# Optimization experiments

Measured on AMD Instinct MI355X. Metric: run time of the kernel, lower is better.

Reference implementation:

```python
import jax, jax.numpy as jnp
import numpy as np

B, T, L, H = 32, 16, 2, 1024  # batch, unroll steps, stacked lstm cells, hidden=input size


def setup_inputs() -> dict:
    key = jax.random.key(0)
    ks = jax.random.split(key, 10)
    s = 1.0 / float(np.sqrt(H))  # torch LSTMCell init scale
    x = jax.random.normal(ks[0], (B, H), jnp.float32)
    h0 = jax.random.normal(ks[1], (L, B, H), jnp.float32)
    c0 = jax.random.normal(ks[2], (L, B, H), jnp.float32)
    # binary zoneout masks (1 -> keep previous state), rate 0.5
    h_mask = (jax.random.uniform(ks[3], (T, L, B, H)) < 0.5).astype(jnp.float32)
    c_mask = (jax.random.uniform(ks[4], (T, L, B, H)) < 0.5).astype(jnp.float32)
    labels = jax.random.normal(ks[5], (B, T, H), jnp.float32)
    W_ih = jax.random.uniform(ks[6], (L, 4 * H, H), jnp.float32, -s, s)
    W_hh = jax.random.uniform(ks[7], (L, 4 * H, H), jnp.float32, -s, s)
    b_ih = jax.random.uniform(ks[8], (L, 4 * H), jnp.float32, -s, s)
    b_hh = jax.random.uniform(ks[9], (L, 4 * H), jnp.float32, -s, s)
    return dict(x=x, h0=h0, c0=c0, h_mask=h_mask, c_mask=c_mask, labels=labels,
                W_ih=W_ih, W_hh=W_hh, b_ih=b_ih, b_hh=b_hh)


def _lstm_cell(x, h, c, W_ih, W_hh, b_ih, b_hh):
    # torch.nn.LSTMCell gate order: i, f, g, o
    gates = x @ W_ih.T + b_ih + h @ W_hh.T + b_hh  # (B, 4H)
    i, f, g, o = jnp.split(gates, 4, axis=-1)
    c_new = jax.nn.sigmoid(f) * c + jax.nn.sigmoid(i) * jnp.tanh(g)
    h_new = jax.nn.sigmoid(o) * jnp.tanh(c_new)
    return h_new, c_new


def reference(x, h0, c0, h_mask, c_mask, labels, W_ih, W_hh, b_ih, b_hh):
    def step(carry, masks):
        hs, cs, out = carry  # hs/cs: (L,B,H), out: (B,H)
        hm, cm = masks       # (L,B,H) each
        new_h, new_c = [], []
        for l in range(L):  # small fixed layer loop (structurally distinct weights)
            h_cand, c_cand = _lstm_cell(out, hs[l], cs[l], W_ih[l], W_hh[l], b_ih[l], b_hh[l])
            # zoneout: mask==1 keeps previous state
            h_l = hm[l] * hs[l] + (1.0 - hm[l]) * h_cand
            c_l = cm[l] * cs[l] + (1.0 - cm[l]) * c_cand
            new_h.append(h_l)
            new_c.append(c_l)
            out = h_l
        return (jnp.stack(new_h), jnp.stack(new_c), out), out

    _, outs = jax.lax.scan(step, (h0, c0, x), (h_mask, c_mask))  # outs: (T,B,H)
    ret = jnp.transpose(outs, (1, 0, 2))  # (B,T,H) == torch.stack(ret, dim=1)
    loss = jnp.mean((ret - labels) ** 2)  # MSELoss
    return ret, loss
```

## Files before the change

### kernel.cpp

```cpp
#include <hip/hip_runtime.h>

#define NTHR 512

typedef __bf16 bf16x8 __attribute__((ext_vector_type(8)));
typedef float  f32x4  __attribute__((ext_vector_type(4)));
typedef unsigned long long u64;

__device__ __forceinline__ unsigned short f2bf(float f) {
  unsigned int u = __float_as_uint(f);
  return (unsigned short)((u + 0x7fffu + ((u >> 16) & 1u)) >> 16);
}
__device__ __forceinline__ bf16x8 asbf(uint4 u) { return __builtin_bit_cast(bf16x8, u); }
__device__ __forceinline__ uint4 mk4(u64 lo, u64 hi) {
  uint2 l = __builtin_bit_cast(uint2, lo), h = __builtin_bit_cast(uint2, hi);
  return make_uint4(l.x, l.y, h.x, h.y);
}
__device__ __forceinline__ float sigf(float xv) { return 1.0f / (1.0f + __expf(-xv)); }

template <typename T>
__device__ __forceinline__ T ald(const T* p) {
  return __hip_atomic_load(p, __ATOMIC_RELAXED, __HIP_MEMORY_SCOPE_AGENT);
}
template <typename T>
__device__ __forceinline__ void xst(T* p, T v) {
  (void)__hip_atomic_exchange(p, v, __ATOMIC_RELAXED, __HIP_MEMORY_SCOPE_AGENT);
}
__device__ __forceinline__ u64 pkf2(float a, float b) {
  float2 f = make_float2(a, b);
  return __builtin_bit_cast(u64, f);
}

#define WS_OUTB 0
#define WS_HBB  131072
#define WS_XFLG 393216
#define WS_HFLG 655360
#define WS_PS   917504
#define WS_BCB  3014656
#define WS_SSE  3047424

__global__ void prep_kernel(const float* __restrict__ x, const float* __restrict__ h0,
                            const float* __restrict__ bih, const float* __restrict__ bhh,
                            unsigned char* __restrict__ ws)
{
  unsigned short* outb = (unsigned short*)(ws + WS_OUTB);
  unsigned short* hbb  = (unsigned short*)(ws + WS_HBB);
  int*   flg = (int*)(ws + WS_XFLG);
  float* bcb = (float*)(ws + WS_BCB);
  float* sse = (float*)(ws + WS_SSE);

  int gid = blockIdx.x * blockDim.x + threadIdx.x;
  int stride = gridDim.x * blockDim.x;

  for (int i = gid; i < 32768; i += stride) outb[i] = f2bf(x[i]);
  for (int i = gid; i < 65536; i += stride) hbb[i] = f2bf(h0[i]);
  for (int i = gid; i < 8192; i += stride) bcb[i] = bih[i] + bhh[i];
  for (int i = gid; i < 131072; i += stride) flg[i] = 0;
  if (gid == 0) *sse = 0.0f;
}

__global__ void __launch_bounds__(NTHR, 1)
lstm_kernel(const float* __restrict__ Wih, const float* __restrict__ Whh,
            const float* __restrict__ h0c, const float* __restrict__ c0c,
            const float* __restrict__ hmask, const float* __restrict__ cmask,
            const float* __restrict__ labels, float* __restrict__ out,
            unsigned char* __restrict__ ws)
{
  const int tid = threadIdx.x, bid = blockIdx.x;
  const int g = bid >> 1, role = bid & 1;
  const int lane = tid & 63, w = tid >> 6;
  const int mt = w & 1, nt = (w >> 1) & 1, kh = w >> 2;
  const int q = lane >> 4, m0 = lane & 15;

  __shared__ __align__(16) unsigned short As[41 * 1032];
  __shared__ __align__(16) float Cred[2][32][36];

  unsigned short* outb = (unsigned short*)(ws + WS_OUTB);
  unsigned short* hbb  = (unsigned short*)(ws + WS_HBB);
  int*   xflg = (int*)(ws + WS_XFLG);
  int*   hflg = (int*)(ws + WS_HFLG);
  float* PsF  = (float*)(ws + WS_PS);
  const float* bcb = (const float*)(ws + WS_BCB);
  float* sse = (float*)(ws + WS_SSE);

  uint4 w0r[16], w1r[16];
  {
    const int nloc = nt * 16 + m0;
    const size_t wrow = (size_t)((nloc >> 3) * 1024 + g * 8 + (nloc & 7));
    const int kbase = kh * 512 + q * 8;
    const float* b0 = (role ? Whh : Wih) + wrow * 1024 + kbase;
    const float* b1 = b0 + 4194304;
#pragma unroll
    for (int ks = 0; ks < 16; ++ks) {
      float4 a = *(const float4*)(b0 + ks * 32), b = *(const float4*)(b0 + ks * 32 + 4);
      w0r[ks].x = (unsigned int)f2bf(a.x) | ((unsigned int)f2bf(a.y) << 16);
      w0r[ks].y = (unsigned int)f2bf(a.z) | ((unsigned int)f2bf(a.w) << 16);
      w0r[ks].z = (unsigned int)f2bf(b.x) | ((unsigned int)f2bf(b.y) << 16);
      w0r[ks].w = (unsigned int)f2bf(b.z) | ((unsigned int)f2bf(b.w) << 16);
      float4 c = *(const float4*)(b1 + ks * 32), d = *(const float4*)(b1 + ks * 32 + 4);
      w1r[ks].x = (unsigned int)f2bf(c.x) | ((unsigned int)f2bf(c.y) << 16);
      w1r[ks].y = (unsigned int)f2bf(c.z) | ((unsigned int)f2bf(c.w) << 16);
      w1r[ks].z = (unsigned int)f2bf(d.x) | ((unsigned int)f2bf(d.y) << 16);
      w1r[ks].w = (unsigned int)f2bf(d.z) | ((unsigned int)f2bf(d.w) << 16);
    }
  }

  const int m = tid >> 3, jc = tid & 7, col = g * 8 + jc;
  float cs0 = 0.f, hs0 = 0.f, cs1 = 0.f, hs1 = 0.f;
  float bv0[4] = {0, 0, 0, 0}, bv1[4] = {0, 0, 0, 0};
  if (role == 0 && tid < 256) {
    cs0 = c0c[m * 1024 + col];           hs0 = h0c[m * 1024 + col];
    cs1 = c0c[32768 + m * 1024 + col];   hs1 = h0c[32768 + m * 1024 + col];
#pragma unroll
    for (int gt = 0; gt < 4; ++gt) {
      bv0[gt] = bcb[gt * 1024 + col];
      bv1[gt] = bcb[4096 + gt * 1024 + col];
    }
  }

#pragma unroll 1
  for (int ci = 0; ci < 32; ++ci) {
    const int t = ci >> 1, L = ci & 1;

    if (role == 0) {
      float hmv = 0.f, cmv = 0.f, lbv = 0.f;
      if (tid < 256) {
        const int mb = ci * 32768 + m * 1024 + col;
        hmv = hmask[mb]; cmv = cmask[mb];
        if (L == 1) lbv = labels[(m * 16 + t) * 1024 + col];
      }

      if (ci > 0 && tid < 128) {
        while (ald(&xflg[((ci - 1) * 128 + tid) * 16]) < ci)
          __builtin_amdgcn_s_sleep(1);
      }
      if (tid >= 128 && tid < 192) {
        while (ald(&hflg[(ci * 128 + g) * 16]) < ci + 1)
          __builtin_amdgcn_s_sleep(1);
      }
      __syncthreads();

      float psv[4];
      const float* psb = PsF + (size_t)(((t & 1) * 2 + L) * 128 + g) * 1024;
      if (tid < 256) {
#pragma unroll
        for (int gt = 0; gt < 4; ++gt)
          psv[gt] = ald(psb + m * 32 + gt * 8 + jc);
      }

      const unsigned short* asrc = outb + L * 32768;
      u64 av[16];
#pragma unroll
      for (int it = 0; it < 16; ++it) {
        const int u = it * 512 + tid, row = u >> 8, c4 = u & 255;
        av[it] = ald((const u64*)(asrc + row * 1024 + c4 * 4));
      }
#pragma unroll
      for (int it = 0; it < 16; ++it) {
        const int u = it * 512 + tid, row = u >> 8, c4 = u & 255;
        *(u64*)&As[row * 1032 + c4 * 4] = av[it];
      }
      __syncthreads();

      f32x4 acc = {0.f, 0.f, 0.f, 0.f};
#pragma unroll
      for (int ks = 0; ks < 16; ++ks) {
        const int kl = kh * 512 + ks * 32 + q * 8;
        bf16x8 a = asbf(*(const uint4*)&As[(mt * 16 + m0) * 1032 + kl]);
        bf16x8 b = asbf((L == 0) ? w0r[ks] : w1r[ks]);
        acc = __builtin_amdgcn_mfma_f32_16x16x32_bf16(a, b, acc, 0, 0, 0);
      }
#pragma unroll
      for (int i = 0; i < 4; ++i)
        Cred[kh][mt * 16 + q * 4 + i][nt * 16 + m0] = acc[i];
      __syncthreads();

      if (tid < 256) {
        float ga[4];
        if (L == 0) {
#pragma unroll
          for (int gt = 0; gt < 4; ++gt)
            ga[gt] = (Cred[0][m][gt * 8 + jc] + Cred[1][m][gt * 8 + jc]) + psv[gt] + bv0[gt];
        } else {
#pragma unroll
          for (int gt = 0; gt < 4; ++gt)
            ga[gt] = (Cred[0][m][gt * 8 + jc] + Cred[1][m][gt * 8 + jc]) + psv[gt] + bv1[gt];
        }
        const float cp = (L == 0) ? cs0 : cs1;
        const float hp = (L == 0) ? hs0 : hs1;
        const float ii = sigf(ga[0]), ff = sigf(ga[1]);
        const float gv = tanhf(ga[2]), oo = sigf(ga[3]);
        const float cc = ff * cp + ii * gv;
        const float hc = oo * tanhf(cc);
        const float hn = hmv * hp + (1.0f - hmv) * hc;
        const float cn = cmv * cp + (1.0f - cmv) * cc;
        if (L == 0) { cs0 = cn; hs0 = hn; } else { cs1 = cn; hs1 = hn; }

        const float hnp = __shfl_xor(hn, 1);
        if ((tid & 1) == 0) {
          const unsigned int hb =
              (unsigned int)f2bf(hn) | ((unsigned int)f2bf(hnp) << 16);
          xst((unsigned int*)&outb[(L ^ 1) * 32768 + m * 1024 + col], hb);
          xst((unsigned int*)&hbb[(((t + 1) & 1) * 2 + L) * 32768 + m * 1024 + col], hb);
        }
        if (L == 1) {
          out[(m * 16 + t) * 1024 + col] = hn;
          float d = hn - lbv;
          float s = d * d;
#pragma unroll
          for (int off = 32; off > 0; off >>= 1) s += __shfl_down(s, off);
          if ((tid & 63) == 0) atomicAdd(sse, s);
        }
      }
      __syncthreads();
      if (tid == 0) xst(&xflg[(ci * 128 + g) * 16], ci + 1);

    } else {
      if (ci > 1 && tid < 128) {
        while (ald(&xflg[((ci - 2) * 128 + tid) * 16]) < ci - 1)
          __builtin_amdgcn_s_sleep(1);
      }
      __syncthreads();

      const unsigned short* asrc = hbb + ((t & 1) * 2 + L) * 32768;
      u64 av[16];
#pragma unroll
      for (int it = 0; it < 16; ++it) {
        const int u = it * 512 + tid, row = u >> 8, c4 = u & 255;
        av[it] = ald((const u64*)(asrc + row * 1024 + c4 * 4));
      }
#pragma unroll
      for (int it = 0; it < 16; ++it) {
        const int u = it * 512 + tid, row = u >> 8, c4 = u & 255;
        *(u64*)&As[row * 1032 + c4 * 4] = av[it];
      }
      __syncthreads();

      f32x4 acc = {0.f, 0.f, 0.f, 0.f};
#pragma unroll
      for (int ks = 0; ks < 16; ++ks) {
        const int kl = kh * 512 + ks * 32 + q * 8;
        bf16x8 a = asbf(*(const uint4*)&As[(mt * 16 + m0) * 1032 + kl]);
        bf16x8 b = asbf((L == 0) ? w0r[ks] : w1r[ks]);
        acc = __builtin_amdgcn_mfma_f32_16x16x32_bf16(a, b, acc, 0, 0, 0);
      }
#pragma unroll
      for (int i = 0; i < 4; ++i)
        Cred[kh][mt * 16 + q * 4 + i][nt * 16 + m0] = acc[i];
      __syncthreads();

      {
        const int mH = tid >> 4, np = tid & 15;
        const float s0 = Cred[0][mH][2 * np]     + Cred[1][mH][2 * np];
        const float s1 = Cred[0][mH][2 * np + 1] + Cred[1][mH][2 * np + 1];
        float* psb = PsF + (size_t)(((t & 1) * 2 + L) * 128 + g) * 1024;
        xst((u64*)(psb + mH * 32 + 2 * np), pkf2(s0, s1));
      }
      __syncthreads();
      if (tid == 0) xst(&hflg[(ci * 128 + g) * 16], ci + 1);
    }
  }
}

__global__ void fin_kernel(float* __restrict__ out, unsigned char* __restrict__ ws) {
  if (blockIdx.x == 0 && threadIdx.x == 0)
    out[524288] = *(float*)(ws + WS_SSE) * (1.0f / 524288.0f);
}

extern "C" void kernel_launch(void* const* d_in, const int* in_sizes, int n_in,
                              void* d_out, int out_size, void* d_ws, size_t ws_size,
                              hipStream_t stream) {
  (void)in_sizes; (void)n_in; (void)out_size; (void)ws_size;
  const float* x   = (const float*)d_in[0];
  const float* h0  = (const float*)d_in[1];
  const float* c0  = (const float*)d_in[2];
  const float* hm  = (const float*)d_in[3];
  const float* cm  = (const float*)d_in[4];
  const float* lb  = (const float*)d_in[5];
  const float* wih = (const float*)d_in[6];
  const float* whh = (const float*)d_in[7];
  const float* bi  = (const float*)d_in[8];
  const float* bh  = (const float*)d_in[9];
  float* out = (float*)d_out;
  unsigned char* ws = (unsigned char*)d_ws;

  prep_kernel<<<dim3(256), dim3(256), 0, stream>>>(x, h0, bi, bh, ws);
  lstm_kernel<<<dim3(256), dim3(NTHR), 0, stream>>>(wih, whh, h0, c0, hm, cm, lb, out, ws);
  fin_kernel<<<dim3(1), dim3(64), 0, stream>>>(out, ws);
}
```

Before: 382.5 us.

## Assign blocks per layer and fuse input and recurrent GEMMs in-block

Work is split across blocks by layer (L = bid&1) instead of by role (input GEMM vs. recurrent-partial GEMM). Each block keeps both its W_ih and W_hh slices in registers. It computes the recurrent partial for the next step locally into shared memory once all blocks have published h. This removes the global partial-sum buffer and the second flag array, but each block now runs two serial GEMMs per step. Layers 0 and 1 can pipeline as a wavefront, with an extra grid-wide wait before each recurrent GEMM.

Result: faster. 343.1 us (-10.3%).

```diff
diff --git a/kernel.cpp b/kernel.cpp
--- a/kernel.cpp
+++ b/kernel.cpp
@@ -11,10 +11,6 @@
   return (unsigned short)((u + 0x7fffu + ((u >> 16) & 1u)) >> 16);
 }
 __device__ __forceinline__ bf16x8 asbf(uint4 u) { return __builtin_bit_cast(bf16x8, u); }
-__device__ __forceinline__ uint4 mk4(u64 lo, u64 hi) {
-  uint2 l = __builtin_bit_cast(uint2, lo), h = __builtin_bit_cast(uint2, hi);
-  return make_uint4(l.x, l.y, h.x, h.y);
-}
 __device__ __forceinline__ float sigf(float xv) { return 1.0f / (1.0f + __expf(-xv)); }
 
 template <typename T>
@@ -25,37 +21,66 @@
 __device__ __forceinline__ void xst(T* p, T v) {
   (void)__hip_atomic_exchange(p, v, __ATOMIC_RELAXED, __HIP_MEMORY_SCOPE_AGENT);
 }
-__device__ __forceinline__ u64 pkf2(float a, float b) {
-  float2 f = make_float2(a, b);
-  return __builtin_bit_cast(u64, f);
-}
-
-#define WS_OUTB 0
-#define WS_HBB  131072
-#define WS_XFLG 393216
-#define WS_HFLG 655360
-#define WS_PS   917504
-#define WS_BCB  3014656
-#define WS_SSE  3047424
+
+#define WS_HOUT 0
+#define WS_XIN  262144
+#define WS_HI0  327680
+#define WS_HI1  393216
+#define WS_FLG  458752
+#define WS_BCB  720896
+#define WS_SSE  753664
 
 __global__ void prep_kernel(const float* __restrict__ x, const float* __restrict__ h0,
                             const float* __restrict__ bih, const float* __restrict__ bhh,
                             unsigned char* __restrict__ ws)
 {
-  unsigned short* outb = (unsigned short*)(ws + WS_OUTB);
-  unsigned short* hbb  = (unsigned short*)(ws + WS_HBB);
-  int*   flg = (int*)(ws + WS_XFLG);
+  unsigned short* xin = (unsigned short*)(ws + WS_XIN);
+  unsigned short* hi0 = (unsigned short*)(ws + WS_HI0);
+  unsigned short* hi1 = (unsigned short*)(ws + WS_HI1);
+  int*   flg = (int*)(ws + WS_FLG);
   float* bcb = (float*)(ws + WS_BCB);
   float* sse = (float*)(ws + WS_SSE);
 
   int gid = blockIdx.x * blockDim.x + threadIdx.x;
   int stride = gridDim.x * blockDim.x;
 
-  for (int i = gid; i < 32768; i += stride) outb[i] = f2bf(x[i]);
-  for (int i = gid; i < 65536; i += stride) hbb[i] = f2bf(h0[i]);
+  for (int i = gid; i < 32768; i += stride) xin[i] = f2bf(x[i]);
+  for (int i = gid; i < 32768; i += stride) hi0[i] = f2bf(h0[i]);
+  for (int i = gid; i < 32768; i += stride) hi1[i] = f2bf(h0[32768 + i]);
   for (int i = gid; i < 8192; i += stride) bcb[i] = bih[i] + bhh[i];
-  for (int i = gid; i < 131072; i += stride) flg[i] = 0;
+  for (int i = gid; i < 65536; i += stride) flg[i] = 0;
   if (gid == 0) *sse = 0.0f;
+}
+
+__device__ __forceinline__ void stage64k(const unsigned short* __restrict__ src,
+                                         unsigned short* __restrict__ As, int tid) {
+  u64 av[16];
+#pragma unroll
+  for (int it = 0; it < 16; ++it) {
+    const int u = it * 512 + tid, row = u >> 8, c4 = u & 255;
+    av[it] = ald((const u64*)(src + row * 1024 + c4 * 4));
+  }
+#pragma unroll
+  for (int it = 0; it < 16; ++it) {
+    const int u = it * 512 + tid, row = u >> 8, c4 = u & 255;
+    *(u64*)&As[row * 1032 + c4 * 4] = av[it];
+  }
+}
+
+__device__ __forceinline__ void gemm_to_cred(const uint4 (&wreg)[16],
+                                             const unsigned short* __restrict__ As,
+                                             float* __restrict__ Cred,
+                                             int mt, int nt, int kh, int q, int m0) {
+  f32x4 acc = {0.f, 0.f, 0.f, 0.f};
+#pragma unroll
+  for (int ks = 0; ks < 16; ++ks) {
+    const int kl = kh * 512 + ks * 32 + q * 8;
+    bf16x8 a = asbf(*(const uint4*)&As[(mt * 16 + m0) * 1032 + kl]);
+    acc = __builtin_amdgcn_mfma_f32_16x16x32_bf16(a, asbf(wreg[ks]), acc, 0, 0, 0);
+  }
+#pragma unroll
+  for (int i = 0; i < 4; ++i)
+    Cred[kh * (32 * 36) + (mt * 16 + q * 4 + i) * 36 + nt * 16 + m0] = acc[i];
 }
 
 __global__ void __launch_bounds__(NTHR, 1)
@@ -66,197 +91,133 @@
             unsigned char* __restrict__ ws)
 {
   const int tid = threadIdx.x, bid = blockIdx.x;
-  const int g = bid >> 1, role = bid & 1;
+  const int L = bid & 1, g = bid >> 1;
   const int lane = tid & 63, w = tid >> 6;
   const int mt = w & 1, nt = (w >> 1) & 1, kh = w >> 2;
   const int q = lane >> 4, m0 = lane & 15;
 
   __shared__ __align__(16) unsigned short As[41 * 1032];
-  __shared__ __align__(16) float Cred[2][32][36];
-
-  unsigned short* outb = (unsigned short*)(ws + WS_OUTB);
-  unsigned short* hbb  = (unsigned short*)(ws + WS_HBB);
-  int*   xflg = (int*)(ws + WS_XFLG);
-  int*   hflg = (int*)(ws + WS_HFLG);
-  float* PsF  = (float*)(ws + WS_PS);
+  __shared__ __align__(16) float Cred[2 * 32 * 36];
+  __shared__ __align__(16) float Hpart[32][33];
+
+  unsigned short* HOUT = (unsigned short*)(ws + WS_HOUT);
+  unsigned short* XIN  = (unsigned short*)(ws + WS_XIN);
+  unsigned short* HIL  = (unsigned short*)(ws + (L ? WS_HI1 : WS_HI0));
+  int*   flg = (int*)(ws + WS_FLG);
   const float* bcb = (const float*)(ws + WS_BCB);
   float* sse = (float*)(ws + WS_SSE);
 
-  uint4 w0r[16], w1r[16];
+  uint4 wx[16], wh[16];
   {
     const int nloc = nt * 16 + m0;
     const size_t wrow = (size_t)((nloc >> 3) * 1024 + g * 8 + (nloc & 7));
     const int kbase = kh * 512 + q * 8;
-    const float* b0 = (role ? Whh : Wih) + wrow * 1024 + kbase;
-    const float* b1 = b0 + 4194304;
+    const float* bx = Wih + (size_t)L * 4194304 + wrow * 1024 + kbase;
+    const float* bh = Whh + (size_t)L * 4194304 + wrow * 1024 + kbase;
 #pragma unroll
     for (int ks = 0; ks < 16; ++ks) {
-      float4 a = *(const float4*)(b0 + ks * 32), b = *(const float4*)(b0 + ks * 32 + 4);
-      w0r[ks].x = (unsigned int)f2bf(a.x) | ((unsigned int)f2bf(a.y) << 16);
-      w0r[ks].y = (unsigned int)f2bf(a.z) | ((unsigned int)f2bf(a.w) << 16);
-      w0r[ks].z = (unsigned int)f2bf(b.x) | ((unsigned int)f2bf(b.y) << 16);
-      w0r[ks].w = (unsigned int)f2bf(b.z) | ((unsigned int)f2bf(b.w) << 16);
-      float4 c = *(const float4*)(b1 + ks * 32), d = *(const float4*)(b1 + ks * 32 + 4);
-      w1r[ks].x = (unsigned int)f2bf(c.x) | ((unsigned int)f2bf(c.y) << 16);
-      w1r[ks].y = (unsigned int)f2bf(c.z) | ((unsigned int)f2bf(c.w) << 16);
-      w1r[ks].z = (unsigned int)f2bf(d.x) | ((unsigned int)f2bf(d.y) << 16);
-      w1r[ks].w = (unsigned int)f2bf(d.z) | ((unsigned int)f2bf(d.w) << 16);
+      float4 a = *(const float4*)(bx + ks * 32), b = *(const float4*)(bx + ks * 32 + 4);
+      wx[ks].x = (unsigned int)f2bf(a.x) | ((unsigned int)f2bf(a.y) << 16);
+      wx[ks].y = (unsigned int)f2bf(a.z) | ((unsigned int)f2bf(a.w) << 16);
+      wx[ks].z = (unsigned int)f2bf(b.x) | ((unsigned int)f2bf(b.y) << 16);
+      wx[ks].w = (unsigned int)f2bf(b.z) | ((unsigned int)f2bf(b.w) << 16);
+      float4 c = *(const float4*)(bh + ks * 32), d = *(const float4*)(bh + ks * 32 + 4);
+      wh[ks].x = (unsigned int)f2bf(c.x) | ((unsigned int)f2bf(c.y) << 16);
+      wh[ks].y = (unsigned int)f2bf(c.z) | ((unsigned int)f2bf(c.w) << 16);
+      wh[ks].z = (unsigned int)f2bf(d.x) | ((unsigned int)f2bf(d.y) << 16);
+      wh[ks].w = (unsigned int)f2bf(d.z) | ((unsigned int)f2bf(d.w) << 16);
     }
   }
 
   const int m = tid >> 3, jc = tid & 7, col = g * 8 + jc;
-  float cs0 = 0.f, hs0 = 0.f, cs1 = 0.f, hs1 = 0.f;
-  float bv0[4] = {0, 0, 0, 0}, bv1[4] = {0, 0, 0, 0};
-  if (role == 0 && tid < 256) {
-    cs0 = c0c[m * 1024 + col];           hs0 = h0c[m * 1024 + col];
-    cs1 = c0c[32768 + m * 1024 + col];   hs1 = h0c[32768 + m * 1024 + col];
-#pragma unroll
-    for (int gt = 0; gt < 4; ++gt) {
-      bv0[gt] = bcb[gt * 1024 + col];
-      bv1[gt] = bcb[4096 + gt * 1024 + col];
-    }
+  float cs = 0.f, hs = 0.f, bv[4] = {0.f, 0.f, 0.f, 0.f};
+  if (tid < 256) {
+    cs = c0c[L * 32768 + m * 1024 + col];
+    hs = h0c[L * 32768 + m * 1024 + col];
+#pragma unroll
+    for (int gt = 0; gt < 4; ++gt) bv[gt] = bcb[L * 4096 + gt * 1024 + col];
+  }
+
+  stage64k(HIL, As, tid);
+  __syncthreads();
+  gemm_to_cred(wh, As, Cred, mt, nt, kh, q, m0);
+  __syncthreads();
+  {
+    const int idx = tid * 2, mh = idx >> 5, nh = idx & 31;
+    Hpart[mh][nh]     = Cred[mh * 36 + nh]     + Cred[32 * 36 + mh * 36 + nh];
+    Hpart[mh][nh + 1] = Cred[mh * 36 + nh + 1] + Cred[32 * 36 + mh * 36 + nh + 1];
   }
 
 #pragma unroll 1
-  for (int ci = 0; ci < 32; ++ci) {
-    const int t = ci >> 1, L = ci & 1;
-
-    if (role == 0) {
-      float hmv = 0.f, cmv = 0.f, lbv = 0.f;
-      if (tid < 256) {
-        const int mb = ci * 32768 + m * 1024 + col;
-        hmv = hmask[mb]; cmv = cmask[mb];
-        if (L == 1) lbv = labels[(m * 16 + t) * 1024 + col];
+  for (int t = 0; t < 16; ++t) {
+    const int ci = 2 * t + L;
+
+    float hmv = 0.f, cmv = 0.f, lbv = 0.f;
+    if (tid < 256) {
+      const int mb = ci * 32768 + m * 1024 + col;
+      hmv = hmask[mb]; cmv = cmask[mb];
+      if (L == 1) lbv = labels[(m * 16 + t) * 1024 + col];
+    }
+
+    if (ci > 0 && tid < 128) {
+      while (ald(&flg[((ci - 1) * 128 + tid) * 16]) < ci)
+        __builtin_amdgcn_s_sleep(1);
+    }
+    __syncthreads();
+
+    const unsigned short* xsrc = (ci == 0)
+        ? XIN
+        : HOUT + (size_t)((L == 0) ? (2 + ((t - 1) & 1)) : (t & 1)) * 32768;
+    stage64k(xsrc, As, tid);
+    __syncthreads();
+
+    gemm_to_cred(wx, As, Cred, mt, nt, kh, q, m0);
+    __syncthreads();
+
+    if (tid < 256) {
+      float ga[4];
+#pragma unroll
+      for (int gt = 0; gt < 4; ++gt)
+        ga[gt] = Cred[m * 36 + gt * 8 + jc] + Cred[32 * 36 + m * 36 + gt * 8 + jc]
+               + Hpart[m][gt * 8 + jc] + bv[gt];
+      const float ii = sigf(ga[0]), ff = sigf(ga[1]);
+      const float gv = tanhf(ga[2]), oo = sigf(ga[3]);
+      const float cc = ff * cs + ii * gv;
+      const float hc = oo * tanhf(cc);
+      const float hn = hmv * hs + (1.0f - hmv) * hc;
+      const float cn = cmv * cs + (1.0f - cmv) * cc;
+      cs = cn; hs = hn;
+
+      const float hnp = __shfl_xor(hn, 1);
+      if (!(tid & 1)) {
+        const unsigned int hb = (unsigned int)f2bf(hn) | ((unsigned int)f2bf(hnp) << 16);
+        xst((unsigned int*)&HOUT[(size_t)(L * 2 + (t & 1)) * 32768 + m * 1024 + col], hb);
       }
-
-      if (ci > 0 && tid < 128) {
-        while (ald(&xflg[((ci - 1) * 128 + tid) * 16]) < ci)
-          __builtin_amdgcn_s_sleep(1);
+      if (L == 1) {
+        out[(m * 16 + t) * 1024 + col] = hn;
+        float d = hn - lbv;
+        float s = d * d;
+#pragma unroll
+        for (int off = 32; off > 0; off >>= 1) s += __shfl_down(s, off);
+        if ((tid & 63) == 0) atomicAdd(sse, s);
       }
-      if (tid >= 128 && tid < 192) {
-        while (ald(&hflg[(ci * 128 + g) * 16]) < ci + 1)
+    }
+    __syncthreads();
+    if (tid == 0) xst(&flg[(ci * 128 + g) * 16], ci + 1);
+
+    if (t < 15) {
+      if (tid < 128) {
+        while (ald(&flg[(ci * 128 + tid) * 16]) < ci + 1)
           __builtin_amdgcn_s_sleep(1);
       }
       __syncthreads();
-
-      float psv[4];
-      const float* psb = PsF + (size_t)(((t & 1) * 2 + L) * 128 + g) * 1024;
-      if (tid < 256) {
-#pragma unroll
-        for (int gt = 0; gt < 4; ++gt)
-          psv[gt] = ald(psb + m * 32 + gt * 8 + jc);
-      }
-
-      const unsigned short* asrc = outb + L * 32768;
-      u64 av[16];
-#pragma unroll
-      for (int it = 0; it < 16; ++it) {
-        const int u = it * 512 + tid, row = u >> 8, c4 = u & 255;
-        av[it] = ald((const u64*)(asrc + row * 1024 + c4 * 4));
-      }
-#pragma unroll
-      for (int it = 0; it < 16; ++it) {
-        const int u = it * 512 + tid, row = u >> 8, c4 = u & 255;
-        *(u64*)&As[row * 1032 + c4 * 4] = av[it];
-      }
+      stage64k(HOUT + (size_t)(L * 2 + (t & 1)) * 32768, As, tid);
       __syncthreads();
-
-      f32x4 acc = {0.f, 0.f, 0.f, 0.f};
-#pragma unroll
-      for (int ks = 0; ks < 16; ++ks) {
-        const int kl = kh * 512 + ks * 32 + q * 8;
-        bf16x8 a = asbf(*(const uint4*)&As[(mt * 16 + m0) * 1032 + kl]);
-        bf16x8 b = asbf((L == 0) ? w0r[ks] : w1r[ks]);
-        acc = __builtin_amdgcn_mfma_f32_16x16x32_bf16(a, b, acc, 0, 0, 0);
-      }
-#pragma unroll
-      for (int i = 0; i < 4; ++i)
-        Cred[kh][mt * 16 + q * 4 + i][nt * 16 + m0] = acc[i];
+      gemm_to_cred(wh, As, Cred, mt, nt, kh, q, m0);
       __syncthreads();
-
-      if (tid < 256) {
-        float ga[4];
-        if (L == 0) {
-#pragma unroll
-          for (int gt = 0; gt < 4; ++gt)
-            ga[gt] = (Cred[0][m][gt * 8 + jc] + Cred[1][m][gt * 8 + jc]) + psv[gt] + bv0[gt];
-        } else {
-#pragma unroll
-          for (int gt = 0; gt < 4; ++gt)
-            ga[gt] = (Cred[0][m][gt * 8 + jc] + Cred[1][m][gt * 8 + jc]) + psv[gt] + bv1[gt];
-        }
-        const float cp = (L == 0) ? cs0 : cs1;
-        const float hp = (L == 0) ? hs0 : hs1;
-        const float ii = sigf(ga[0]), ff = sigf(ga[1]);
-        const float gv = tanhf(ga[2]), oo = sigf(ga[3]);
-        const float cc = ff * cp + ii * gv;
-        const float hc = oo * tanhf(cc);
-        const float hn = hmv * hp + (1.0f - hmv) * hc;
-        const float cn = cmv * cp + (1.0f - cmv) * cc;
-        if (L == 0) { cs0 = cn; hs0 = hn; } else { cs1 = cn; hs1 = hn; }
-
-        const float hnp = __shfl_xor(hn, 1);
-        if ((tid & 1) == 0) {
-          const unsigned int hb =
-              (unsigned int)f2bf(hn) | ((unsigned int)f2bf(hnp) << 16);
-          xst((unsigned int*)&outb[(L ^ 1) * 32768 + m * 1024 + col], hb);
-          xst((unsigned int*)&hbb[(((t + 1) & 1) * 2 + L) * 32768 + m * 1024 + col], hb);
-        }
-        if (L == 1) {
-          out[(m * 16 + t) * 1024 + col] = hn;
-          float d = hn - lbv;
-          float s = d * d;
-#pragma unroll
-          for (int off = 32; off > 0; off >>= 1) s += __shfl_down(s, off);
-          if ((tid & 63) == 0) atomicAdd(sse, s);
-        }
-      }
-      __syncthreads();
-      if (tid == 0) xst(&xflg[(ci * 128 + g) * 16], ci + 1);
-
-    } else {
-      if (ci > 1 && tid < 128) {
-        while (ald(&xflg[((ci - 2) * 128 + tid) * 16]) < ci - 1)
-          __builtin_amdgcn_s_sleep(1);
-      }
-      __syncthreads();
-
-      const unsigned short* asrc = hbb + ((t & 1) * 2 + L) * 32768;
-      u64 av[16];
-#pragma unroll
-      for (int it = 0; it < 16; ++it) {
-        const int u = it * 512 + tid, row = u >> 8, c4 = u & 255;
-        av[it] = ald((const u64*)(asrc + row * 1024 + c4 * 4));
-      }
-#pragma unroll
-      for (int it = 0; it < 16; ++it) {
-        const int u = it * 512 + tid, row = u >> 8, c4 = u & 255;
-        *(u64*)&As[row * 1032 + c4 * 4] = av[it];
-      }
-      __syncthreads();
-
-      f32x4 acc = {0.f, 0.f, 0.f, 0.f};
-#pragma unroll
-      for (int ks = 0; ks < 16; ++ks) {
-        const int kl = kh * 512 + ks * 32 + q * 8;
-        bf16x8 a = asbf(*(const uint4*)&As[(mt * 16 + m0) * 1032 + kl]);
-        bf16x8 b = asbf((L == 0) ? w0r[ks] : w1r[ks]);
-        acc = __builtin_amdgcn_mfma_f32_16x16x32_bf16(a, b, acc, 0, 0, 0);
-      }
-#pragma unroll
-      for (int i = 0; i < 4; ++i)
-        Cred[kh][mt * 16 + q * 4 + i][nt * 16 + m0] = acc[i];
-      __syncthreads();
-
-      {
-        const int mH = tid >> 4, np = tid & 15;
-        const float s0 = Cred[0][mH][2 * np]     + Cred[1][mH][2 * np];
-        const float s1 = Cred[0][mH][2 * np + 1] + Cred[1][mH][2 * np + 1];
-        float* psb = PsF + (size_t)(((t & 1) * 2 + L) * 128 + g) * 1024;
-        xst((u64*)(psb + mH * 32 + 2 * np), pkf2(s0, s1));
-      }
-      __syncthreads();
-      if (tid == 0) xst(&hflg[(ci * 128 + g) * 16], ci + 1);
+      const int idx = tid * 2, mh = idx >> 5, nh = idx & 31;
+      Hpart[mh][nh]     = Cred[mh * 36 + nh]     + Cred[32 * 36 + mh * 36 + nh];
+      Hpart[mh][nh + 1] = Cred[mh * 36 + nh + 1] + Cred[32 * 36 + mh * 36 + nh + 1];
     }
   }
 }
```
